# Performance work log

Measured on AMD Instinct MI355X. Metric: run time of the kernel, lower is better.

## Reference

```python
import jax, jax.numpy as jnp
import numpy as np

N_HEADS = 8
ITER = 3


def setup_inputs() -> dict:
    key = jax.random.key(0)
    ks = jax.random.split(key, 9)
    B, L, D = 2, 2048, 512
    s = 1.0 / np.sqrt(D)
    return {
        "queries": jax.random.normal(ks[0], (B, L, D), jnp.float32),
        "keys": jax.random.normal(ks[1], (B, L, D), jnp.float32),
        "values": jax.random.normal(ks[2], (B, L, D), jnp.float32),
        "Wq": jax.random.normal(ks[3], (D, D), jnp.float32) * s,
        "bq": jax.random.normal(ks[4], (D,), jnp.float32) * s,
        "Wk": jax.random.normal(ks[5], (D, D), jnp.float32) * s,
        "bk": jax.random.normal(ks[6], (D,), jnp.float32) * s,
        "Wv": jax.random.normal(ks[7], (D, D), jnp.float32) * s,
        "bv": jax.random.normal(ks[8], (D,), jnp.float32) * s,
    }


def reference(queries, keys, values, Wq, bq, Wk, bk, Wv, bv):
    B, L, D = queries.shape
    S = keys.shape[1]
    H = N_HEADS
    E = D // H
    q = (queries @ Wq + bq).reshape(B, L, H, E)
    k = (keys @ Wk + bk).reshape(B, S, H, E)
    v = (values @ Wv + bv).reshape(B, S, H, E)

    attn_list = []
    vals_accum = jnp.zeros((B, S, H, E), dtype=q.dtype)
    for i in range(ITER):
        stride = i + 1
        tmp_q = q[:, ::stride]  # (B, L_i, H, E) strided query gather
        attn = jnp.einsum('blhe,bshe->bhls', tmp_q, k)  # (B,H,L_i,S)
        attn_list.append(attn)
        att = jax.nn.softmax(attn, axis=-1)
        # dropout is identity in eval mode
        # 'bhls,bshe->bshe' == values scaled by column-sum of attention over l
        colsum = att.sum(axis=2)  # (B,H,S)
        vals_accum = vals_accum + v * colsum.transpose(0, 2, 1)[..., None]
    final_values = vals_accum / ITER  # mean over the ITER branches
    out = final_values.reshape(B, S, H * E)
    return (out, *attn_list)
```

## Files before the change

### kernel.cpp

```cpp
#include <hip/hip_runtime.h>


typedef short s16x8 __attribute__((ext_vector_type(8)));
typedef float f32x4 __attribute__((ext_vector_type(4)));
typedef unsigned short u16;
typedef unsigned short u16x4 __attribute__((ext_vector_type(4)));

#define MFMA16(a, b, c) __builtin_amdgcn_mfma_f32_16x16x32_bf16((a), (b), (c), 0, 0, 0)

__device__ __forceinline__ u16 f32_to_bf16(float f) {
  unsigned u = __builtin_bit_cast(unsigned, f);
  unsigned r = u + 0x7fffu + ((u >> 16) & 1u);
  return (u16)(r >> 16);
}
__device__ __forceinline__ void split1(float x, u16& h, u16& l) {
  h = f32_to_bf16(x);
  l = f32_to_bf16(x - __builtin_bit_cast(float, (unsigned)h << 16));
}

__global__ __launch_bounds__(256) void split_all(const float* __restrict__ in_q,
                                                 const float* __restrict__ in_k,
                                                 const float* __restrict__ in_v,
                                                 const float* __restrict__ Wq,
                                                 const float* __restrict__ Wk,
                                                 const float* __restrict__ Wv,
                                                 u16* __restrict__ Xsplit,
                                                 u16* __restrict__ Wsplit) {
  int which = blockIdx.y;
  int bx = blockIdx.x;
  if (bx < 1024) {
    const float* X = (which == 0) ? in_q : (which == 1) ? in_k : in_v;
    u16* Xh = Xsplit + (size_t)which * 2 * 2097152;
    u16* Xl = Xh + 2097152;
    int t = bx * 256 + threadIdx.x;
    int lane = t & 63;
    int kc = (t >> 6) & 15;
    int mt = t >> 10;
    int lr = lane & 15, g = lane >> 4;
    const float* p = X + (size_t)(mt * 16 + lr) * 512 + kc * 32 + g * 8;
    float4 a = *(const float4*)p;
    float4 b = *(const float4*)(p + 4);
    float x[8] = {a.x, a.y, a.z, a.w, b.x, b.y, b.z, b.w};
    s16x8 hv, lv;
#pragma unroll
    for (int j = 0; j < 8; ++j) {
      u16 hh, ll;
      split1(x[j], hh, ll);
      hv[j] = (short)hh;
      lv[j] = (short)ll;
    }
    size_t off = (size_t)t * 8;
    *(s16x8*)(Xh + off) = hv;
    *(s16x8*)(Xl + off) = lv;
  } else {
    const float* W = (which == 0) ? Wq : (which == 1) ? Wk : Wv;
    u16* Wh = Wsplit + (size_t)which * 2 * 262144;
    u16* Wl = Wh + 262144;
    int t = (bx - 1024) * 256 + threadIdx.x;
    int lane = t & 63;
    int kc = (t >> 6) & 15;
    int nt = t >> 10;
    int lr = lane & 15, g = lane >> 4;
    s16x8 hv, lv;
#pragma unroll
    for (int j = 0; j < 8; ++j) {
      float x = W[(size_t)(kc * 32 + g * 8 + j) * 512 + nt * 16 + lr];
      u16 hh, ll;
      split1(x, hh, ll);
      hv[j] = (short)hh;
      lv[j] = (short)ll;
    }
    size_t off = (size_t)t * 8;
    *(s16x8*)(Wh + off) = hv;
    *(s16x8*)(Wl + off) = lv;
  }
}

__global__ __launch_bounds__(256) void proj_gemm3(const u16* __restrict__ Xsplit,
                                                  const u16* __restrict__ Wsplit,
                                                  const float* __restrict__ bq,
                                                  const float* __restrict__ bk,
                                                  const float* __restrict__ bv,
                                                  float* __restrict__ vout,
                                                  u16* __restrict__ qh,
                                                  u16* __restrict__ ql,
                                                  u16* __restrict__ kh,
                                                  u16* __restrict__ kl) {
  int z = blockIdx.z;
  const u16* Xh = Xsplit + (size_t)z * 2 * 2097152;
  const u16* Xl = Xh + 2097152;
  const u16* Wh = Wsplit + (size_t)z * 2 * 262144;
  const u16* Wl = Wh + 262144;
  const float* bias = (z == 0) ? bq : (z == 1) ? bk : bv;
  u16* Yhi = (z == 0) ? qh : kh;
  u16* Ylo = (z == 0) ? ql : kl;

  int tid = threadIdx.x;
  int wid = tid >> 6, lane = tid & 63;
  int wr = wid >> 1, wc = wid & 1;
  int mtb = blockIdx.y * 4 + wr * 2;
  int ntb = blockIdx.x * 4 + wc * 2;

  f32x4 zero = {0.f, 0.f, 0.f, 0.f};
  f32x4 acc[2][2];
#pragma unroll
  for (int m = 0; m < 2; ++m)
#pragma unroll
    for (int n = 0; n < 2; ++n) acc[m][n] = zero;

  for (int kc = 0; kc < 16; ++kc) {
    s16x8 xh[2], xl[2], wh[2], wl[2];
#pragma unroll
    for (int m = 0; m < 2; ++m) {
      size_t off = ((size_t)((mtb + m) * 16 + kc) * 64 + lane) * 8;
      xh[m] = *(const s16x8*)(Xh + off);
      xl[m] = *(const s16x8*)(Xl + off);
    }
#pragma unroll
    for (int n = 0; n < 2; ++n) {
      size_t off = ((size_t)((ntb + n) * 16 + kc) * 64 + lane) * 8;
      wh[n] = *(const s16x8*)(Wh + off);
      wl[n] = *(const s16x8*)(Wl + off);
    }
#pragma unroll
    for (int m = 0; m < 2; ++m)
#pragma unroll
      for (int n = 0; n < 2; ++n) {
        acc[m][n] = MFMA16(wh[n], xh[m], acc[m][n]);
        acc[m][n] = MFMA16(wh[n], xl[m], acc[m][n]);
        acc[m][n] = MFMA16(wl[n], xh[m], acc[m][n]);
      }
  }
  int cn = lane & 15, rg = lane >> 4;
#pragma unroll
  for (int m = 0; m < 2; ++m) {
    int row = (mtb + m) * 16 + cn;
#pragma unroll
    for (int n = 0; n < 2; ++n) {
      int nc0 = (ntb + n) * 16 + rg * 4;
      f32x4 b4 = *(const f32x4*)(bias + nc0);
      f32x4 y;
#pragma unroll
      for (int r = 0; r < 4; ++r) y[r] = acc[m][n][r] + b4[r];
      if (z == 2) {
        *(f32x4*)(vout + (size_t)row * 512 + nc0) = y;
      } else {
        int b = row >> 11, l = row & 2047;
        int h = nc0 >> 6;
        int e0 = nc0 & 63;
        int bh2 = b * 8 + h;
        int lt = l >> 4, lr2 = l & 15;
        int kc2 = e0 >> 5, g2 = (e0 >> 3) & 3, j0 = e0 & 7;
        size_t idx = ((((size_t)bh2 * 128 + lt) * 2 + kc2) * 64 + g2 * 16 + lr2) * 8 + j0;
        u16x4 hv, lv;
#pragma unroll
        for (int r = 0; r < 4; ++r) {
          u16 hh, ll;
          split1(y[r], hh, ll);
          hv[r] = hh;
          lv[r] = ll;
        }
        *(u16x4*)(Yhi + idx) = hv;
        *(u16x4*)(Ylo + idx) = lv;
      }
    }
  }
}

__global__ __launch_bounds__(512, 4) void attn_fused(const u16* __restrict__ qh,
                                                     const u16* __restrict__ ql,
                                                     const u16* __restrict__ kh,
                                                     const u16* __restrict__ kl,
                                                     float* __restrict__ a1,
                                                     float* __restrict__ a2,
                                                     float* __restrict__ a3,
                                                     float* __restrict__ partials) {
  int wg = blockIdx.x;
  int xcd = wg & 7;
  int idx = wg >> 3;
  int bh = xcd * 2 + (idx >> 7);
  int lblk = idx & 127;
  int tid = threadIdx.x, wid = tid >> 6, lane = tid & 63;

  s16x8 qhf[2], qlf[2];
#pragma unroll
  for (int kc = 0; kc < 2; ++kc) {
    size_t off = ((((size_t)bh * 128 + lblk) * 2 + kc) * 64 + lane) * 8;
    qhf[kc] = *(const s16x8*)(qh + off);
    qlf[kc] = *(const s16x8*)(ql + off);
  }

  f32x4 acc[16];
#pragma unroll
  for (int t = 0; t < 16; ++t) acc[t] = (f32x4){0.f, 0.f, 0.f, 0.f};

#pragma unroll
  for (int t = 0; t < 16; ++t) {
    int st = wid * 16 + t;
#pragma unroll
    for (int kc = 0; kc < 2; ++kc) {
      size_t off = ((((size_t)bh * 128 + st) * 2 + kc) * 64 + lane) * 8;
      s16x8 khf = *(const s16x8*)(kh + off);
      s16x8 klf = *(const s16x8*)(kl + off);
      acc[t] = MFMA16(qhf[kc], khf, acc[t]);
      acc[t] = MFMA16(qhf[kc], klf, acc[t]);
      acc[t] = MFMA16(qlf[kc], khf, acc[t]);
    }
  }

  int cn = lane & 15, rg = lane >> 4;
  int lbase = lblk * 16;
  float* A1 = a1 + (size_t)bh * 2048 * 2048;
  float* A2 = a2 + (size_t)bh * 1024 * 2048;
  float* A3 = a3 + (size_t)bh * 683 * 2048;
#pragma unroll
  for (int r = 0; r < 4; ++r) {
    int l = lbase + rg * 4 + r;
    float* p1 = A1 + (size_t)l * 2048 + wid * 256 + cn;
#pragma unroll
    for (int t = 0; t < 16; ++t) __builtin_nontemporal_store(acc[t][r], p1 + t * 16);
    if ((l & 1) == 0) {
      float* p2 = A2 + (size_t)(l >> 1) * 2048 + wid * 256 + cn;
#pragma unroll
      for (int t = 0; t < 16; ++t) __builtin_nontemporal_store(acc[t][r], p2 + t * 16);
    }
    if (l % 3 == 0) {
      float* p3 = A3 + (size_t)(l / 3) * 2048 + wid * 256 + cn;
#pragma unroll
      for (int t = 0; t < 16; ++t) __builtin_nontemporal_store(acc[t][r], p3 + t * 16);
    }
  }

  __shared__ float lred[16][8];
  float mrow[4];
#pragma unroll
  for (int r = 0; r < 4; ++r) {
    float m = acc[0][r];
#pragma unroll
    for (int t = 1; t < 16; ++t) m = fmaxf(m, acc[t][r]);
#pragma unroll
    for (int o = 1; o < 16; o <<= 1) m = fmaxf(m, __shfl_xor(m, o));
    mrow[r] = m;
  }
  if (cn == 0) {
#pragma unroll
    for (int r = 0; r < 4; ++r) lred[rg * 4 + r][wid] = mrow[r];
  }
  __syncthreads();
  float mfin[4];
#pragma unroll
  for (int r = 0; r < 4; ++r) {
    int rr = rg * 4 + r;
    float m = lred[rr][0];
#pragma unroll
    for (int w = 1; w < 8; ++w) m = fmaxf(m, lred[rr][w]);
    mfin[r] = m;
  }
  __syncthreads();

  float zrow[4] = {0.f, 0.f, 0.f, 0.f};
#pragma unroll
  for (int t = 0; t < 16; ++t) {
#pragma unroll
    for (int r = 0; r < 4; ++r) {
      float p = __expf(acc[t][r] - mfin[r]);
      acc[t][r] = p;
      zrow[r] += p;
    }
  }
#pragma unroll
  for (int r = 0; r < 4; ++r) {
#pragma unroll
    for (int o = 1; o < 16; o <<= 1) zrow[r] += __shfl_xor(zrow[r], o);
  }
  if (cn == 0) {
#pragma unroll
    for (int r = 0; r < 4; ++r) lred[rg * 4 + r][wid] = zrow[r];
  }
  __syncthreads();
  float winv[4];
#pragma unroll
  for (int r = 0; r < 4; ++r) {
    int rr = rg * 4 + r;
    int l = lbase + rr;
    float zs = lred[rr][0];
#pragma unroll
    for (int w = 1; w < 8; ++w) zs += lred[rr][w];
    float w_ = 1.f + (((l & 1) == 0) ? 1.f : 0.f) + ((l % 3 == 0) ? 1.f : 0.f);
    winv[r] = w_ / zs;
  }

  __shared__ float pcol[2048];
#pragma unroll
  for (int t = 0; t < 16; ++t) {
    float cs = acc[t][0] * winv[0] + acc[t][1] * winv[1] + acc[t][2] * winv[2] +
               acc[t][3] * winv[3];
    cs += __shfl_xor(cs, 16);
    cs += __shfl_xor(cs, 32);
    if (lane < 16) pcol[wid * 256 + t * 16 + cn] = cs;
  }
  __syncthreads();
  size_t pb = ((size_t)bh * 128 + lblk) * 2048;
  *(f32x4*)&partials[pb + tid * 4] = *(const f32x4*)&pcol[tid * 4];
}

__global__ __launch_bounds__(256) void reduce_partials(const float* __restrict__ partials,
                                                       float* __restrict__ csum) {
  int s = blockIdx.x * 256 + threadIdx.x;
  int bh = blockIdx.y;
  float acc = 0.f;
  for (int j = 0; j < 128; ++j) acc += partials[((size_t)(bh * 128 + j)) * 2048 + s];
  csum[(size_t)bh * 2048 + s] = acc;
}

__global__ __launch_bounds__(256) void final_out(const float* __restrict__ v,
                                                 const float* __restrict__ csum,
                                                 float* __restrict__ out) {
  int idx = blockIdx.x * 256 + threadIdx.x;
  int h = (idx >> 4) & 7;
  int s = (idx >> 7) & 2047;
  int b = idx >> 18;
  float4 vv = ((const float4*)v)[idx];
  float c = csum[(size_t)(b * 8 + h) * 2048 + s] * (1.f / 3.f);
  float4 o = {vv.x * c, vv.y * c, vv.z * c, vv.w * c};
  ((float4*)out)[idx] = o;
}

extern "C" void kernel_launch(void* const* d_in, const int* in_sizes, int n_in,
                              void* d_out, int out_size, void* d_ws, size_t ws_size,
                              hipStream_t stream) {
  const float* queries = (const float*)d_in[0];
  const float* keys    = (const float*)d_in[1];
  const float* values  = (const float*)d_in[2];
  const float* Wq = (const float*)d_in[3];
  const float* bq = (const float*)d_in[4];
  const float* Wk = (const float*)d_in[5];
  const float* bk = (const float*)d_in[6];
  const float* Wv = (const float*)d_in[7];
  const float* bv = (const float*)d_in[8];

  float* out = (float*)d_out;
  float* a1 = out + 2097152;
  float* a2 = a1 + 67108864;
  float* a3 = a2 + 33554432;

  float* ws = (float*)d_ws;
  float* v = ws;
  u16* qh = (u16*)(v + 2097152);
  u16* ql = qh + 2097152;
  u16* kh = ql + 2097152;
  u16* kl = kh + 2097152;
  u16* Wsplit = kl + 2097152;
  u16* Xsplit = Wsplit + 6 * 262144;
  float* partials = (float*)Xsplit;
  float* csum = (float*)Wsplit;

  split_all<<<dim3(1152, 3), 256, 0, stream>>>(queries, keys, values, Wq, Wk, Wv,
                                               Xsplit, Wsplit);

  proj_gemm3<<<dim3(8, 64, 3), 256, 0, stream>>>(Xsplit, Wsplit, bq, bk, bv, v,
                                                 qh, ql, kh, kl);

  attn_fused<<<dim3(2048), 512, 0, stream>>>(qh, ql, kh, kl, a1, a2, a3, partials);

  reduce_partials<<<dim3(8, 16), 256, 0, stream>>>(partials, csum);

  final_out<<<dim3(2048), 256, 0, stream>>>(v, csum, out);
}
```

Baseline: 193.4 us.

## Split attention-score stores into separate recompute kernel using 32x32 MFMA tiles

Removes the three attention-matrix stores from the fused softmax/colsum kernel, which now only produces column-sum partials. A new kernel recomputes QK^T with 32x32x16 bf16 MFMA tiles (3-pass hi/lo split) and writes the A1/A2/A3 outputs with nontemporal stores, where each lane's 16 accumulator values share a column. The goal is a lighter stats kernel and a store-dedicated kernel whose write pattern may suit memory better, at the cost of computing QK^T twice and adding a launch.

```diff
diff --git a/kernel.cpp b/kernel.cpp
--- a/kernel.cpp
+++ b/kernel.cpp
@@ -3,10 +3,12 @@
 
 typedef short s16x8 __attribute__((ext_vector_type(8)));
 typedef float f32x4 __attribute__((ext_vector_type(4)));
+typedef float f32x16 __attribute__((ext_vector_type(16)));
 typedef unsigned short u16;
 typedef unsigned short u16x4 __attribute__((ext_vector_type(4)));
 
 #define MFMA16(a, b, c) __builtin_amdgcn_mfma_f32_16x16x32_bf16((a), (b), (c), 0, 0, 0)
+#define MFMA32(a, b, c) __builtin_amdgcn_mfma_f32_32x32x16_bf16((a), (b), (c), 0, 0, 0)
 
 __device__ __forceinline__ u16 f32_to_bf16(float f) {
   unsigned u = __builtin_bit_cast(unsigned, f);
@@ -167,13 +169,10 @@
   }
 }
 
-__global__ __launch_bounds__(512, 4) void attn_fused(const u16* __restrict__ qh,
+__global__ __launch_bounds__(512, 4) void attn_stats(const u16* __restrict__ qh,
                                                      const u16* __restrict__ ql,
                                                      const u16* __restrict__ kh,
                                                      const u16* __restrict__ kl,
-                                                     float* __restrict__ a1,
-                                                     float* __restrict__ a2,
-                                                     float* __restrict__ a3,
                                                      float* __restrict__ partials) {
   int wg = blockIdx.x;
   int xcd = wg & 7;
@@ -210,26 +209,6 @@
 
   int cn = lane & 15, rg = lane >> 4;
   int lbase = lblk * 16;
-  float* A1 = a1 + (size_t)bh * 2048 * 2048;
-  float* A2 = a2 + (size_t)bh * 1024 * 2048;
-  float* A3 = a3 + (size_t)bh * 683 * 2048;
-#pragma unroll
-  for (int r = 0; r < 4; ++r) {
-    int l = lbase + rg * 4 + r;
-    float* p1 = A1 + (size_t)l * 2048 + wid * 256 + cn;
-#pragma unroll
-    for (int t = 0; t < 16; ++t) __builtin_nontemporal_store(acc[t][r], p1 + t * 16);
-    if ((l & 1) == 0) {
-      float* p2 = A2 + (size_t)(l >> 1) * 2048 + wid * 256 + cn;
-#pragma unroll
-      for (int t = 0; t < 16; ++t) __builtin_nontemporal_store(acc[t][r], p2 + t * 16);
-    }
-    if (l % 3 == 0) {
-      float* p3 = A3 + (size_t)(l / 3) * 2048 + wid * 256 + cn;
-#pragma unroll
-      for (int t = 0; t < 16; ++t) __builtin_nontemporal_store(acc[t][r], p3 + t * 16);
-    }
-  }
 
   __shared__ float lred[16][8];
   float mrow[4];
@@ -302,6 +281,74 @@
   __syncthreads();
   size_t pb = ((size_t)bh * 128 + lblk) * 2048;
   *(f32x4*)&partials[pb + tid * 4] = *(const f32x4*)&pcol[tid * 4];
+}
+
+__global__ __launch_bounds__(256, 4) void attn_store(const u16* __restrict__ qh,
+                                                     const u16* __restrict__ ql,
+                                                     const u16* __restrict__ kh,
+                                                     const u16* __restrict__ kl,
+                                                     float* __restrict__ a1,
+                                                     float* __restrict__ a2,
+                                                     float* __restrict__ a3) {
+  int wg = blockIdx.x;
+  int xcd = wg & 7;
+  int idx = wg >> 3;
+  int bh = xcd * 2 + (idx >> 6);
+  int lblk = idx & 63;
+  int tid = threadIdx.x, wid = tid >> 6, lane = tid & 63;
+  int qbase = lblk * 32;
+  int row32 = lane & 31, hi = lane >> 5, lr = lane & 15;
+
+  s16x8 aqh[4], aql[4];
+  {
+    int lt = (qbase + row32) >> 4;
+#pragma unroll
+    for (int c = 0; c < 4; ++c) {
+      int e0 = c * 16 + hi * 8;
+      int kc2 = e0 >> 5, g2 = (e0 >> 3) & 3;
+      size_t off = ((((size_t)bh * 128 + lt) * 2 + kc2) * 64 + g2 * 16 + lr) * 8;
+      aqh[c] = *(const s16x8*)(qh + off);
+      aql[c] = *(const s16x8*)(ql + off);
+    }
+  }
+
+  float* A1 = a1 + (size_t)bh * 2048 * 2048;
+  float* A2 = a2 + (size_t)bh * 1024 * 2048;
+  float* A3 = a3 + (size_t)bh * 683 * 2048;
+
+  for (int t = 0; t < 16; ++t) {
+    int sbase = wid * 512 + t * 32;
+    s16x8 bkh[4], bkl[4];
+    int ltk = (sbase + row32) >> 4;
+#pragma unroll
+    for (int c = 0; c < 4; ++c) {
+      int e0 = c * 16 + hi * 8;
+      int kc2 = e0 >> 5, g2 = (e0 >> 3) & 3;
+      size_t off = ((((size_t)bh * 128 + ltk) * 2 + kc2) * 64 + g2 * 16 + lr) * 8;
+      bkh[c] = *(const s16x8*)(kh + off);
+      bkl[c] = *(const s16x8*)(kl + off);
+    }
+    f32x16 acc;
+#pragma unroll
+    for (int i = 0; i < 16; ++i) acc[i] = 0.f;
+#pragma unroll
+    for (int c = 0; c < 4; ++c) {
+      acc = MFMA32(aqh[c], bkh[c], acc);
+      acc = MFMA32(aqh[c], bkl[c], acc);
+      acc = MFMA32(aql[c], bkh[c], acc);
+    }
+#pragma unroll
+    for (int r = 0; r < 16; ++r) {
+      int rq = (r & 3) + 8 * (r >> 2) + 4 * hi;
+      int l = qbase + rq;
+      size_t co = (size_t)sbase + row32;
+      __builtin_nontemporal_store(acc[r], A1 + (size_t)l * 2048 + co);
+      if ((r & 1) == 0)
+        __builtin_nontemporal_store(acc[r], A2 + (size_t)(l >> 1) * 2048 + co);
+      if (l % 3 == 0)
+        __builtin_nontemporal_store(acc[r], A3 + (size_t)(l / 3) * 2048 + co);
+    }
+  }
 }
 
 __global__ __launch_bounds__(256) void reduce_partials(const float* __restrict__ partials,
@@ -361,9 +408,11 @@
   proj_gemm3<<<dim3(8, 64, 3), 256, 0, stream>>>(Xsplit, Wsplit, bq, bk, bv, v,
                                                  qh, ql, kh, kl);
 
-  attn_fused<<<dim3(2048), 512, 0, stream>>>(qh, ql, kh, kl, a1, a2, a3, partials);
+  attn_stats<<<dim3(2048), 512, 0, stream>>>(qh, ql, kh, kl, partials);
 
   reduce_partials<<<dim3(8, 16), 256, 0, stream>>>(partials, csum);
 
   final_out<<<dim3(2048), 256, 0, stream>>>(v, csum, out);
-}
+
+  attn_store<<<dim3(1024), 256, 0, stream>>>(qh, ql, kh, kl, a1, a2, a3);
+}
```

New measurement: 227.6 us. 1.18x slower.
